# Kernel optimization log

Measured on AMD Instinct MI355X. Metric: run time of the kernel, lower is better.

## Reference

```python
import jax, jax.numpy as jnp
import numpy as np

D = 128; H = 4; HD = 32; K = 4; OUT = 2; COND = 6; FF = 256

def _ln(x, g, b):
    m = x.mean(-1, keepdims=True)
    v = ((x - m) ** 2).mean(-1, keepdims=True)
    return g * (x - m) * jax.lax.rsqrt(v + 1e-5) + b

def setup_inputs() -> dict:
    key = jax.random.key(0)
    ks = jax.random.split(key, 40)
    B, S = 4096, 128
    def w(k, shape, scale=0.05):
        return (jax.random.normal(k, shape, dtype=jnp.float32) * scale)
    inp = {
        'x': jax.random.normal(ks[0], (B, OUT, S), dtype=jnp.float32),
        'timesteps': jax.random.randint(ks[1], (B,), 0, 1000, dtype=jnp.int32),
        'conditions': jax.random.normal(ks[2], (B, S, COND), dtype=jnp.float32),
        # time embedding MLP: Linear(128->256), SiLU, Linear(256->128)
        't_w1': w(ks[3], (D, 2 * D)), 't_b1': jnp.zeros((2 * D,), jnp.float32),
        't_w2': w(ks[4], (2 * D, D)), 't_b2': jnp.zeros((D,), jnp.float32),
        # condition MLP: Linear(6->64), SiLU, Linear(64->128), SiLU
        'c_w1': w(ks[5], (COND, D // 2)), 'c_b1': jnp.zeros((D // 2,), jnp.float32),
        'c_w2': w(ks[6], (D // 2, D)), 'c_b2': jnp.zeros((D,), jnp.float32),
        # 2 transformer encoder layers (post-norm, relu FFN, dropout=0 eval)
        'attn_wqkv': w(ks[7], (2, D, 3 * D)), 'attn_bqkv': jnp.zeros((2, 3 * D), jnp.float32),
        'attn_wo': w(ks[8], (2, D, D)), 'attn_bo': jnp.zeros((2, D), jnp.float32),
        'ln1_g': jnp.ones((2, D), jnp.float32), 'ln1_b': jnp.zeros((2, D), jnp.float32),
        'ff_w1': w(ks[9], (2, D, FF)), 'ff_b1': jnp.zeros((2, FF), jnp.float32),
        'ff_w2': w(ks[10], (2, FF, D)), 'ff_b2': jnp.zeros((2, D), jnp.float32),
        'ln2_g': jnp.ones((2, D), jnp.float32), 'ln2_b': jnp.zeros((2, D), jnp.float32),
        # mixture weights net: Linear(256->128), SiLU, Linear(128->4), Softmax
        'mw_w1': w(ks[11], (2 * D, D)), 'mw_b1': jnp.zeros((D,), jnp.float32),
        'mw_w2': w(ks[12], (D, K)), 'mw_b2': jnp.zeros((K,), jnp.float32),
        # K student networks: Linear(2+256->128), Tanh, Linear(128->2)
        's_w1': w(ks[13], (K, OUT + 2 * D, D)), 's_b1': jnp.zeros((K, D), jnp.float32),
        's_w2': w(ks[14], (K, D, OUT)), 's_b2': jnp.zeros((K, OUT), jnp.float32),
    }
    return inp

def reference(x, timesteps, conditions, t_w1, t_b1, t_w2, t_b2, c_w1, c_b1, c_w2, c_b2,
              attn_wqkv, attn_bqkv, attn_wo, attn_bo, ln1_g, ln1_b, ff_w1, ff_b1,
              ff_w2, ff_b2, ln2_g, ln2_b, mw_w1, mw_b1, mw_w2, mw_b2,
              s_w1, s_b1, s_w2, s_b2):
    B, _, S = x.shape
    # sinusoidal time embedding
    half = D // 2
    freqs = jnp.exp(-jnp.log(jnp.float32(10000.0)) * jnp.arange(half, dtype=jnp.float32) / half)
    args = timesteps.astype(jnp.float32)[:, None] * freqs[None, :]
    te = jnp.concatenate([jnp.cos(args), jnp.sin(args)], axis=-1)            # [B, D]
    time_emb = jax.nn.silu(te @ t_w1 + t_b1) @ t_w2 + t_b2                   # [B, D]
    # condition embedding MLP
    h = jax.nn.silu(conditions @ c_w1 + c_b1)
    h = jax.nn.silu(h @ c_w2 + c_b2)                                          # [B, S, D]
    # 2-layer transformer encoder (post-norm)
    for l in range(2):
        qkv = h @ attn_wqkv[l] + attn_bqkv[l]                                 # [B, S, 3D]
        q, k, v = jnp.split(qkv, 3, axis=-1)
        q = q.reshape(B, S, H, HD); k = k.reshape(B, S, H, HD); v = v.reshape(B, S, H, HD)
        sc = jnp.einsum('bqhd,bkhd->bhqk', q, k) / jnp.sqrt(jnp.float32(HD))
        a = jax.nn.softmax(sc, axis=-1)
        o = jnp.einsum('bhqk,bkhd->bqhd', a, v).reshape(B, S, D)
        o = o @ attn_wo[l] + attn_bo[l]
        h = _ln(h + o, ln1_g[l], ln1_b[l])
        f = jax.nn.relu(h @ ff_w1[l] + ff_b1[l]) @ ff_w2[l] + ff_b2[l]
        h = _ln(h + f, ln2_g[l], ln2_b[l])
    cond_emb = h.mean(axis=1)                                                 # [B, D]
    combined = jnp.concatenate([time_emb, cond_emb], axis=-1)                 # [B, 2D]
    mw = jax.nn.softmax(jax.nn.silu(combined @ mw_w1 + mw_b1) @ mw_w2 + mw_b2, axis=-1)  # [B, K]
    # students over all seq positions (vectorized over original seq loop)
    xt = jnp.transpose(x, (0, 2, 1))                                          # [B, S, OUT]
    emb_bs = jnp.broadcast_to(combined[:, None, :], (B, S, 2 * D))
    inp = jnp.concatenate([xt, emb_bs], axis=-1)                              # [B, S, OUT+2D]
    hk = jnp.tanh(jnp.einsum('bsi,kio->bsko', inp, s_w1) + s_b1)              # [B, S, K, D]
    ok = jnp.einsum('bsko,koj->bskj', hk, s_w2) + s_b2                        # [B, S, K, OUT]
    out = jnp.einsum('bskj,bk->bsj', ok, mw)                                  # [B, S, OUT]
    return jnp.transpose(out, (0, 2, 1))                                      # [B, OUT, S]
```

## Files before the change

kernel.cpp:

```cpp
#include <hip/hip_runtime.h>

typedef _Float16 hf;
typedef _Float16 hf4 __attribute__((ext_vector_type(4)));
typedef _Float16 hf8 __attribute__((ext_vector_type(8)));
typedef float f4 __attribute__((ext_vector_type(4)));

#define NTH 512
#define ACT_OFF 0
#define P_OFF   32768
#define SC_OFF  40960
#define SMEM_BYTES 73728

#define WSH_QKV 0
#define WSH_WO  98304
#define WSH_FW1 131072
#define WSH_FW2 196608
#define WSH_CW2 262144
#define WSH_TOTAL 270336
#define CEMB_BYTE_OFF 540672

__device__ __forceinline__ float dsilu(float x){ return x / (1.f + __expf(-x)); }
__device__ __forceinline__ float dtanh(float x){
  float xc = fminf(fmaxf(x, -10.f), 10.f);
  float e = __expf(2.f * xc);
  return (e - 1.f) / (e + 1.f);
}

__global__ void prep_pack(const float* __restrict__ wqkv, const float* __restrict__ wo,
                          const float* __restrict__ fw1, const float* __restrict__ fw2,
                          const float* __restrict__ cw2, hf* __restrict__ ws){
  int idx = blockIdx.x * 256 + threadIdx.x;
  if (idx >= WSH_TOTAL) return;
  float v;
  if (idx < WSH_WO){
    int u = idx; int lh = u / 12288; int l = lh >> 2, h = lh & 3;
    int r = u % 12288; int tl = r >> 9; int lane = (r >> 3) & 63; int j = r & 7;
    int q = lane >> 4, c = lane & 15;
    int tn = tl >> 2, tk = tl & 3;
    int k = tk*32 + q*8 + j, nloc = tn*16 + c;
    int gcol = (nloc >> 5)*128 + h*32 + (nloc & 31);
    v = wqkv[l*49152 + k*384 + gcol];
  } else if (idx < WSH_FW1){
    int u = idx - WSH_WO; int l = u >> 14; int r = u & 16383;
    int tl = r >> 9; int lane = (r >> 3) & 63; int j = r & 7;
    int q = lane >> 4, c = lane & 15;
    int tn = tl >> 2, tk = tl & 3;
    v = wo[l*16384 + (tk*32 + q*8 + j)*128 + tn*16 + c];
  } else if (idx < WSH_FW2){
    int u = idx - WSH_FW1; int lch = u >> 14; int l = lch >> 1, ch = lch & 1; int r = u & 16383;
    int tl = r >> 9; int lane = (r >> 3) & 63; int j = r & 7;
    int q = lane >> 4, c = lane & 15;
    int tn = tl >> 2, tk = tl & 3;
    v = fw1[l*32768 + (tk*32 + q*8 + j)*256 + ch*128 + tn*16 + c];
  } else if (idx < WSH_CW2){
    int u = idx - WSH_FW2; int lch = u >> 14; int l = lch >> 1, ch = lch & 1; int r = u & 16383;
    int tl = r >> 9; int lane = (r >> 3) & 63; int j = r & 7;
    int q = lane >> 4, c = lane & 15;
    int tn = tl >> 2, tk = tl & 3;
    v = fw2[l*32768 + (ch*128 + tk*32 + q*8 + j)*128 + tn*16 + c];
  } else {
    int u = idx - WSH_CW2;
    int tl = u >> 9; int lane = (u >> 3) & 63; int j = u & 7;
    int q = lane >> 4, c = lane & 15;
    int tn = tl >> 1, tk = tl & 1;
    v = cw2[(tk*32 + q*8 + j)*128 + tn*16 + c];
  }
  ws[idx] = (hf)v;
}

template<int KT>
__device__ __forceinline__ void gemmB(f4 (&acc)[4][2], const hf* __restrict__ Ag, const hf* Bh,
                                      int npair, int shalf, int lane){
#pragma unroll
  for (int tk = 0; tk < KT; ++tk){
    hf8 a0 = *(const hf8*)(Ag + (((2*npair    )*KT + tk) << 9) + lane*8);
    hf8 a1 = *(const hf8*)(Ag + (((2*npair + 1)*KT + tk) << 9) + lane*8);
#pragma unroll
    for (int si = 0; si < 4; ++si){
      hf8 b = *(const hf8*)(Bh + (((shalf*4 + si)*KT + tk) << 9) + lane*8);
      acc[si][0] = __builtin_amdgcn_mfma_f32_16x16x32_f16(a0, b, acc[si][0], 0, 0, 0);
      acc[si][1] = __builtin_amdgcn_mfma_f32_16x16x32_f16(a1, b, acc[si][1], 0, 0, 0);
    }
  }
}

__device__ __forceinline__ void store_packed_b64(hf* dst, int KtilesOut, int ts, int ft,
                                                 f4 v, int q, int c){
  int tk = ft >> 1;
  int qp = ((ft & 1) << 1) + (q >> 1);
  int j0 = (q & 1) << 2;
  hf4 h; h[0] = (hf)v[0]; h[1] = (hf)v[1]; h[2] = (hf)v[2]; h[3] = (hf)v[3];
  *(hf4*)(dst + ((ts*KtilesOut + tk) << 9) + ((qp*16 + c) << 3) + j0) = h;
}

__device__ __forceinline__ void ln_pass(hf* A, const hf* Dh, const float* __restrict__ g,
                                        const float* __restrict__ bb, int t){
  int s = t >> 2, p = t & 3;
  float xr[4][8];
  int offs[4];
  float sum = 0.f, sq = 0.f;
#pragma unroll
  for (int tk = 0; tk < 4; ++tk){
    int off = (((s >> 4) * 4 + tk) << 9) + ((p * 16 + (s & 15)) << 3);
    offs[tk] = off;
    hf8 va = *(const hf8*)(A + off);
    hf8 vd = *(const hf8*)(Dh + off);
#pragma unroll
    for (int j = 0; j < 8; ++j){
      float x = (float)va[j] + (float)vd[j];
      xr[tk][j] = x; sum += x; sq += x * x;
    }
  }
  sum += __shfl_xor(sum, 1); sq += __shfl_xor(sq, 1);
  sum += __shfl_xor(sum, 2); sq += __shfl_xor(sq, 2);
  float mean = sum * (1.f/128.f);
  float rstd = rsqrtf(sq * (1.f/128.f) - mean*mean + 1e-5f);
#pragma unroll
  for (int tk = 0; tk < 4; ++tk){
    int f0 = tk*32 + p*8;
    f4 g0 = *(const f4*)(g + f0); f4 g1 = *(const f4*)(g + f0 + 4);
    f4 b0 = *(const f4*)(bb + f0); f4 b1 = *(const f4*)(bb + f0 + 4);
    hf8 y;
#pragma unroll
    for (int j = 0; j < 4; ++j){
      y[j]     = (hf)((xr[tk][j]     - mean) * rstd * g0[j] + b0[j]);
      y[j + 4] = (hf)((xr[tk][j + 4] - mean) * rstd * g1[j] + b1[j]);
    }
    *(hf8*)(A + offs[tk]) = y;
  }
}

__global__ __launch_bounds__(NTH, 4) void fused_fp(
    const float* __restrict__ cond,
    const float* __restrict__ c_w1, const float* __restrict__ c_b1, const float* __restrict__ c_b2,
    const float* __restrict__ bqkv_g, const float* __restrict__ bo_g,
    const float* __restrict__ ln1g_g, const float* __restrict__ ln1b_g,
    const float* __restrict__ fb1_g, const float* __restrict__ fb2_g,
    const float* __restrict__ ln2g_g, const float* __restrict__ ln2b_g,
    const hf* __restrict__ wsp, float* __restrict__ cemb)
{
  extern __shared__ char smem[];
  hf* ACTh = (hf*)(smem + ACT_OFF);
  hf* Ph   = (hf*)(smem + P_OFF);
  hf* SCh  = (hf*)(smem + SC_OFF);
  float* SCf = (float*)(smem + SC_OFF);
  hf* Qh  = SCh;
  hf* Kh  = (hf*)(smem + SC_OFF + 8192);
  hf* VTh = (hf*)(smem + SC_OFF + 16384);
  float* cst  = SCf + 4096;
  float* cw1s = SCf + 4864;

  const int b = blockIdx.x;
  const int t = threadIdx.x;
  const int w = t >> 6, lane = t & 63, q = lane >> 4, c = lane & 15;
  const int sp = w & 3, np = w >> 2;
  const int npair = w & 3, shalf = w >> 2;

  for (int idx = t; idx < 768; idx += NTH) cst[idx] = cond[b * 768 + idx];
  if (t < 384) cw1s[t] = c_w1[t];
  if (t < 64)  cw1s[384 + t] = c_b1[t];
  __syncthreads();

  for (int idx = t; idx < 8192; idx += NTH){
    int s = idx >> 6, jf = idx & 63;
    float a = cw1s[384 + jf];
#pragma unroll
    for (int cc = 0; cc < 6; ++cc) a += cst[s * 6 + cc] * cw1s[cc * 64 + jf];
    SCh[(((s >> 4)*2 + (jf >> 5)) << 9) + ((((jf & 31) >> 3)*16 + (s & 15)) << 3) + (jf & 7)] = (hf)dsilu(a);
  }
  __syncthreads();

  {
    f4 acc[4][2];
#pragma unroll
    for (int i = 0; i < 4; ++i)
#pragma unroll
      for (int j = 0; j < 2; ++j){ f4 z = {0.f,0.f,0.f,0.f}; acc[i][j] = z; }
    gemmB<2>(acc, wsp + WSH_CW2, SCh, npair, shalf, lane);
    f4 cb0 = *(const f4*)(c_b2 + (2*npair    )*16 + q*4);
    f4 cb1 = *(const f4*)(c_b2 + (2*npair + 1)*16 + q*4);
#pragma unroll
    for (int si = 0; si < 4; ++si)
#pragma unroll
      for (int jn = 0; jn < 2; ++jn){
        f4 v = acc[si][jn];
        f4 cb = jn ? cb1 : cb0;
#pragma unroll
        for (int r = 0; r < 4; ++r) v[r] = dsilu(v[r] + cb[r]);
        store_packed_b64(ACTh, 4, shalf*4 + si, 2*npair + jn, v, q, c);
      }
  }

  for (int l = 0; l < 2; ++l){
    f4 oacc[8];
#pragma unroll
    for (int i = 0; i < 8; ++i){ f4 z = {0.f,0.f,0.f,0.f}; oacc[i] = z; }

    for (int h = 0; h < 4; ++h){
      __syncthreads();
      {
        const hf* Aq = wsp + WSH_QKV + (l*4 + h)*12288;
        f4 acc[2][3];
#pragma unroll
        for (int i = 0; i < 2; ++i)
#pragma unroll
          for (int j = 0; j < 3; ++j){ f4 z = {0.f,0.f,0.f,0.f}; acc[i][j] = z; }
#pragma unroll
        for (int tk = 0; tk < 4; ++tk){
          hf8 b0 = *(const hf8*)(ACTh + (((2*sp  )*4 + tk) << 9) + lane*8);
          hf8 b1 = *(const hf8*)(ACTh + (((2*sp+1)*4 + tk) << 9) + lane*8);
#pragma unroll
          for (int jn = 0; jn < 3; ++jn){
            hf8 a = *(const hf8*)(Aq + (((np*3 + jn)*4 + tk) << 9) + lane*8);
            acc[0][jn] = __builtin_amdgcn_mfma_f32_16x16x32_f16(a, b0, acc[0][jn], 0, 0, 0);
            acc[1][jn] = __builtin_amdgcn_mfma_f32_16x16x32_f16(a, b1, acc[1][jn], 0, 0, 0);
          }
        }
#pragma unroll
        for (int si = 0; si < 2; ++si)
#pragma unroll
          for (int jn = 0; jn < 3; ++jn){
            int ft = np*3 + jn, ts = 2*sp + si;
            int sel = ft >> 1;
            f4 v = acc[si][jn];
            f4 bq = *(const f4*)(bqkv_g + l*384 + sel*128 + h*32 + (ft & 1)*16 + q*4);
#pragma unroll
            for (int r = 0; r < 4; ++r) v[r] += bq[r];
            if (sel == 0){
#pragma unroll
              for (int r = 0; r < 4; ++r) v[r] *= 0.17677669529663687f;
              store_packed_b64(Qh, 1, ts, ft, v, q, c);
            } else if (sel == 1){
              store_packed_b64(Kh, 1, ts, ft - 2, v, q, c);
            } else {
              int td = ft - 4;
              int qp = ((ts & 1) << 1) + (c >> 3);
              hf* pb = VTh + ((td*4 + (ts >> 1)) << 9) + (c & 7);
#pragma unroll
              for (int r = 0; r < 4; ++r) pb[(qp*16 + q*4 + r) << 3] = (hf)v[r];
            }
          }
      }
      __syncthreads();
      {
        hf8 qf = *(const hf8*)(Qh + (w << 9) + lane*8);
        f4 sc[8];
#pragma unroll
        for (int kst = 0; kst < 8; ++kst){
          hf8 kv = *(const hf8*)(Kh + (kst << 9) + lane*8);
          f4 z = {0.f,0.f,0.f,0.f};
          sc[kst] = __builtin_amdgcn_mfma_f32_16x16x32_f16(kv, qf, z, 0, 0, 0);
        }
        float ls = 0.f;
#pragma unroll
        for (int kst = 0; kst < 8; ++kst)
#pragma unroll
          for (int r = 0; r < 4; ++r){
            float e = __expf(sc[kst][r]);
            sc[kst][r] = e; ls += e;
          }
        ls += __shfl_xor(ls, 16);
        ls += __shfl_xor(ls, 32);
        float rl = 1.f / ls;
        hf* Pw = Ph + (w << 9);
#pragma unroll
        for (int ks = 0; ks < 4; ++ks){
#pragma unroll
          for (int h2 = 0; h2 < 2; ++h2){
            int kst = 2*ks + h2;
            int qp = h2*2 + (q >> 1);
            int j0 = (q & 1) << 2;
            hf4 pv;
#pragma unroll
            for (int r = 0; r < 4; ++r) pv[r] = (hf)(sc[kst][r] * rl);
            *(hf4*)(Pw + qp*128 + c*8 + j0) = pv;
          }
          hf8 bp = *(const hf8*)(Pw + lane*8);
          hf8 a0 = *(const hf8*)(VTh + ((     ks) << 9) + lane*8);
          hf8 a1 = *(const hf8*)(VTh + ((4 +  ks) << 9) + lane*8);
          oacc[2*h]     = __builtin_amdgcn_mfma_f32_16x16x32_f16(a0, bp, oacc[2*h],     0, 0, 0);
          oacc[2*h + 1] = __builtin_amdgcn_mfma_f32_16x16x32_f16(a1, bp, oacc[2*h + 1], 0, 0, 0);
        }
      }
    }

    __syncthreads();
#pragma unroll
    for (int ft = 0; ft < 8; ++ft) store_packed_b64(SCh, 4, w, ft, oacc[ft], q, c);
    __syncthreads();

    {
      f4 acc[4][2];
#pragma unroll
      for (int i = 0; i < 4; ++i)
#pragma unroll
        for (int j = 0; j < 2; ++j){ f4 z = {0.f,0.f,0.f,0.f}; acc[i][j] = z; }
      gemmB<4>(acc, wsp + WSH_WO + l*16384, SCh, npair, shalf, lane);
      __syncthreads();
      f4 bo0 = *(const f4*)(bo_g + l*128 + (2*npair    )*16 + q*4);
      f4 bo1 = *(const f4*)(bo_g + l*128 + (2*npair + 1)*16 + q*4);
#pragma unroll
      for (int si = 0; si < 4; ++si)
#pragma unroll
        for (int jn = 0; jn < 2; ++jn){
          f4 v = acc[si][jn];
          f4 bo = jn ? bo1 : bo0;
#pragma unroll
          for (int r = 0; r < 4; ++r) v[r] += bo[r];
          store_packed_b64(SCh, 4, shalf*4 + si, 2*npair + jn, v, q, c);
        }
    }
    __syncthreads();
    ln_pass(ACTh, SCh, ln1g_g + l*128, ln1b_g + l*128, t);
    __syncthreads();

    {
      f4 facc[4][2];
#pragma unroll
      for (int i = 0; i < 4; ++i)
#pragma unroll
        for (int j = 0; j < 2; ++j){ f4 z = {0.f,0.f,0.f,0.f}; facc[i][j] = z; }
      for (int ch = 0; ch < 2; ++ch){
        f4 acc[4][2];
#pragma unroll
        for (int i = 0; i < 4; ++i)
#pragma unroll
          for (int j = 0; j < 2; ++j){ f4 z = {0.f,0.f,0.f,0.f}; acc[i][j] = z; }
        gemmB<4>(acc, wsp + WSH_FW1 + (l*2 + ch)*16384, ACTh, npair, shalf, lane);
        f4 fb0 = *(const f4*)(fb1_g + l*256 + ch*128 + (2*npair    )*16 + q*4);
        f4 fb1v = *(const f4*)(fb1_g + l*256 + ch*128 + (2*npair + 1)*16 + q*4);
#pragma unroll
        for (int si = 0; si < 4; ++si)
#pragma unroll
          for (int jn = 0; jn < 2; ++jn){
            f4 v = acc[si][jn];
            f4 fb = jn ? fb1v : fb0;
#pragma unroll
            for (int r = 0; r < 4; ++r) v[r] = fmaxf(v[r] + fb[r], 0.f);
            store_packed_b64(SCh, 4, shalf*4 + si, 2*npair + jn, v, q, c);
          }
        __syncthreads();
        gemmB<4>(facc, wsp + WSH_FW2 + (l*2 + ch)*16384, SCh, npair, shalf, lane);
        __syncthreads();
      }
      f4 f20 = *(const f4*)(fb2_g + l*128 + (2*npair    )*16 + q*4);
      f4 f21 = *(const f4*)(fb2_g + l*128 + (2*npair + 1)*16 + q*4);
#pragma unroll
      for (int si = 0; si < 4; ++si)
#pragma unroll
        for (int jn = 0; jn < 2; ++jn){
          f4 v = facc[si][jn];
          f4 fb = jn ? f21 : f20;
#pragma unroll
          for (int r = 0; r < 4; ++r) v[r] += fb[r];
          store_packed_b64(SCh, 4, shalf*4 + si, 2*npair + jn, v, q, c);
        }
    }
    __syncthreads();
    ln_pass(ACTh, SCh, ln2g_g + l*128, ln2b_g + l*128, t);
    __syncthreads();
  }

  {
    int o = t & 15;
    float fs[8];
#pragma unroll
    for (int j = 0; j < 8; ++j) fs[j] = 0.f;
#pragma unroll
    for (int u = 0; u < 4; ++u){
      int s = (t >> 4)*4 + u;
      hf8 v = *(const hf8*)(ACTh + (((s >> 4)*4 + (o >> 2)) << 9) + (((o & 3)*16 + (s & 15)) << 3));
#pragma unroll
      for (int j = 0; j < 8; ++j) fs[j] += (float)v[j];
    }
#pragma unroll
    for (int j = 0; j < 8; ++j){
      fs[j] += __shfl_xor(fs[j], 16);
      fs[j] += __shfl_xor(fs[j], 32);
    }
    if (lane < 16){
      f4 v0, v1;
#pragma unroll
      for (int j = 0; j < 4; ++j){ v0[j] = fs[j]; v1[j] = fs[j+4]; }
      *(f4*)(SCf + w*128 + o*8)     = v0;
      *(f4*)(SCf + w*128 + o*8 + 4) = v1;
    }
  }
  __syncthreads();
  if (t < 128){
    float a = 0.f;
#pragma unroll
    for (int wv = 0; wv < 8; ++wv) a += SCf[wv*128 + t];
    cemb[b*128 + t] = a * (1.f/128.f);
  }
}

__global__ __launch_bounds__(256, 8) void tail_k(
    const float* __restrict__ x, const int* __restrict__ tstep, const float* __restrict__ cemb,
    const float* __restrict__ t_w1, const float* __restrict__ t_b1,
    const float* __restrict__ t_w2, const float* __restrict__ t_b2,
    const float* __restrict__ mw_w1, const float* __restrict__ mw_b1,
    const float* __restrict__ mw_w2, const float* __restrict__ mw_b2,
    const float* __restrict__ s_w1, const float* __restrict__ s_b1,
    const float* __restrict__ s_w2, const float* __restrict__ s_b2,
    float* __restrict__ out)
{
  __shared__ float sw01[1024], sw2[1024];
  __shared__ float comb[256];
  __shared__ float cvec[512];
  __shared__ float scr[1024];
  __shared__ float mwh[128], mwls[4];
  const int b = blockIdx.x;
  const int t = threadIdx.x;

  for (int i = t; i < 1024; i += 256){
    int row = i >> 9, k = (i >> 7) & 3, j = i & 127;
    sw01[i] = s_w1[k*33024 + row*128 + j];
    sw2[i]  = s_w2[i];
  }
  if (t < 128){
    int i = t & 63;
    float f = __expf(-logf(10000.f) * (float)i * (1.f/64.f));
    float a = (float)tstep[b] * f;
    cvec[t] = (t < 64) ? cosf(a) : sinf(a);
    comb[128 + t] = cemb[b*128 + t];
  }
  __syncthreads();

  {
    float a = t_b1[t];
#pragma unroll 8
    for (int i = 0; i < 128; ++i) a += cvec[i] * t_w1[i*256 + t];
    cvec[128 + t] = dsilu(a);
  }
  __syncthreads();

  {
    int ih = t >> 7, j = t & 127;
    float a = ih ? 0.f : t_b2[j];
#pragma unroll 8
    for (int ii = 0; ii < 128; ++ii){
      int i = ih*128 + ii;
      a += cvec[128 + i] * t_w2[i*128 + j];
    }
    scr[t] = a;
  }
  __syncthreads();
  if (t < 128) comb[t] = scr[t] + scr[128 + t];
  __syncthreads();

  {
    int ih = t >> 7, k = (t >> 5) & 3, j4 = t & 31;
    f4 a = {0.f, 0.f, 0.f, 0.f};
    const f4* wp = (const f4*)(s_w1 + k*33024 + 256 + ih*16384) + j4;
#pragma unroll 4
    for (int ii = 0; ii < 128; ++ii){
      float cb = comb[ih*128 + ii];
      f4 wv = wp[ii*32];
      a[0] += cb*wv[0]; a[1] += cb*wv[1]; a[2] += cb*wv[2]; a[3] += cb*wv[3];
    }
    ((f4*)scr)[ih*128 + k*32 + j4] = a;
  }
  __syncthreads();

  if (t < 128){
    f4 r0 = ((f4*)scr)[t];
    f4 r1 = ((f4*)scr)[128 + t];
    f4 r; r[0] = r0[0]+r1[0]; r[1] = r0[1]+r1[1]; r[2] = r0[2]+r1[2]; r[3] = r0[3]+r1[3];
    int k = t >> 5, j4 = t & 31;
    f4 sb = *(const f4*)(s_b1 + k*128 + j4*4);
    r[0] += sb[0]; r[1] += sb[1]; r[2] += sb[2]; r[3] += sb[3];
    ((f4*)cvec)[t] = r;
  } else {
    int j = t - 128;
    float a = mw_b1[j];
#pragma unroll 8
    for (int i = 0; i < 256; ++i) a += comb[i] * mw_w1[i*128 + j];
    mwh[j] = dsilu(a);
  }
  __syncthreads();

  if (t < 64){
    int cc = t & 3, j0 = t >> 2;
    float a = 0.f;
#pragma unroll
    for (int i = 0; i < 8; ++i){
      int j = j0 + 16*i;
      a += mwh[j] * mw_w2[j*4 + cc];
    }
    a += __shfl_xor(a, 4);
    a += __shfl_xor(a, 8);
    a += __shfl_xor(a, 16);
    a += __shfl_xor(a, 32);
    if (t < 4) mwls[t] = a + mw_b2[t];
  }
#pragma unroll
  for (int u = 0; u < 2; ++u){
    int o = t + u*256, k = o >> 7, s = o & 127;
    float x0 = x[b*256 + s];
    float x1 = x[b*256 + 128 + s];
    float a0 = 0.f, a1 = 0.f;
#pragma unroll 4
    for (int j = 0; j < 128; ++j){
      float hk = dtanh(cvec[k*128 + j] + x0*sw01[k*128 + j] + x1*sw01[512 + k*128 + j]);
      a0 += hk * sw2[k*256 + 2*j];
      a1 += hk * sw2[k*256 + 2*j + 1];
    }
    scr[k*256 + s]       = a0 + s_b2[2*k];
    scr[k*256 + 128 + s] = a1 + s_b2[2*k + 1];
  }
  __syncthreads();

  {
    int row = t >> 7, s = t & 127;
    float l0 = mwls[0], l1 = mwls[1], l2 = mwls[2], l3 = mwls[3];
    float mx = fmaxf(fmaxf(l0, l1), fmaxf(l2, l3));
    float e0 = __expf(l0 - mx), e1 = __expf(l1 - mx), e2 = __expf(l2 - mx), e3 = __expf(l3 - mx);
    float rs = 1.f / (e0 + e1 + e2 + e3);
    float a = e0*scr[0*256 + row*128 + s] + e1*scr[1*256 + row*128 + s]
            + e2*scr[2*256 + row*128 + s] + e3*scr[3*256 + row*128 + s];
    out[b*256 + row*128 + s] = a * rs;
  }
}

extern "C" void kernel_launch(void* const* d_in, const int* in_sizes, int n_in,
                              void* d_out, int out_size, void* d_ws, size_t ws_size,
                              hipStream_t stream){
  (void)n_in; (void)ws_size; (void)out_size;
  hipFuncSetAttribute((const void*)fused_fp, hipFuncAttributeMaxDynamicSharedMemorySize, SMEM_BYTES);
  int B = in_sizes[1];
  hf* wsp = (hf*)d_ws;
  float* cemb = (float*)((char*)d_ws + CEMB_BYTE_OFF);
  prep_pack<<<dim3((WSH_TOTAL + 255) / 256), dim3(256), 0, stream>>>(
      (const float*)d_in[11], (const float*)d_in[13], (const float*)d_in[17],
      (const float*)d_in[19], (const float*)d_in[9], wsp);
  fused_fp<<<dim3(B), dim3(NTH), SMEM_BYTES, stream>>>(
      (const float*)d_in[2],
      (const float*)d_in[7], (const float*)d_in[8], (const float*)d_in[10],
      (const float*)d_in[12], (const float*)d_in[14],
      (const float*)d_in[15], (const float*)d_in[16],
      (const float*)d_in[18], (const float*)d_in[20],
      (const float*)d_in[21], (const float*)d_in[22],
      wsp, cemb);
  tail_k<<<dim3(B), dim3(256), 0, stream>>>(
      (const float*)d_in[0], (const int*)d_in[1], cemb,
      (const float*)d_in[3], (const float*)d_in[4], (const float*)d_in[5], (const float*)d_in[6],
      (const float*)d_in[23], (const float*)d_in[24], (const float*)d_in[25], (const float*)d_in[26],
      (const float*)d_in[27], (const float*)d_in[28], (const float*)d_in[29], (const float*)d_in[30],
      (float*)d_out);
}
```

Baseline: 1.088 ms.

## Prefetch MFMA weight fragments before barriers and use fp16 dot2 in tail

In the fused transformer kernel, the global-memory weight fragments for each GEMM are loaded into registers before the preceding __syncthreads. This lets their latency overlap with the barrier wait, and the FFN chunk loop is unrolled so each chunk's loads are issued early. The tail kernel now reads fp16-prepacked time-MLP, mixture and student weights from a new prep kernel and accumulates with dot2 instructions. The student tanh loop is also vectorized with f4 shared-memory reads. This raises register pressure and lowers tail-path precision to fp16 inputs.

```diff
diff --git a/kernel.cpp b/kernel.cpp
--- a/kernel.cpp
+++ b/kernel.cpp
@@ -1,6 +1,7 @@
 #include <hip/hip_runtime.h>
 
 typedef _Float16 hf;
+typedef _Float16 hf2 __attribute__((ext_vector_type(2)));
 typedef _Float16 hf4 __attribute__((ext_vector_type(4)));
 typedef _Float16 hf8 __attribute__((ext_vector_type(8)));
 typedef float f4 __attribute__((ext_vector_type(4)));
@@ -18,12 +19,25 @@
 #define WSH_CW2 262144
 #define WSH_TOTAL 270336
 #define CEMB_BYTE_OFF 540672
+#define SP1_BYTE_OFF  2637824
+#define TPH_SW1 0
+#define TPH_TW1 131072
+#define TPH_TW2 163840
+#define TPH_MW1 196608
+#define TPH_TOTAL 229376
 
 __device__ __forceinline__ float dsilu(float x){ return x / (1.f + __expf(-x)); }
 __device__ __forceinline__ float dtanh(float x){
   float xc = fminf(fmaxf(x, -10.f), 10.f);
   float e = __expf(2.f * xc);
   return (e - 1.f) / (e + 1.f);
+}
+__device__ __forceinline__ float fdot2f(hf2 a, hf2 b, float c){
+#if __has_builtin(__builtin_amdgcn_fdot2)
+  return __builtin_amdgcn_fdot2(a, b, c, false);
+#else
+  return c + (float)a[0]*(float)b[0] + (float)a[1]*(float)b[1];
+#endif
 }
 
 __global__ void prep_pack(const float* __restrict__ wqkv, const float* __restrict__ wo,
@@ -68,18 +82,50 @@
   ws[idx] = (hf)v;
 }
 
+__global__ void prep_pack2(const float* __restrict__ s_w1, const float* __restrict__ t_w1,
+                           const float* __restrict__ t_w2, const float* __restrict__ mw_w1,
+                           hf* __restrict__ sp1){
+  int idx = blockIdx.x * 256 + threadIdx.x;
+  if (idx >= TPH_TOTAL) return;
+  float v;
+  if (idx < TPH_TW1){
+    int par = idx & 1, j = (idx >> 1) & 127, ip = (idx >> 8) & 127, k = idx >> 15;
+    v = s_w1[k*33024 + (2 + 2*ip + par)*128 + j];
+  } else if (idx < TPH_TW2){
+    int u = idx - TPH_TW1;
+    int par = u & 1, tc = (u >> 1) & 255, ip = u >> 9;
+    v = t_w1[(2*ip + par)*256 + tc];
+  } else if (idx < TPH_MW1){
+    int u = idx - TPH_TW2;
+    int par = u & 1, j = (u >> 1) & 127, ip = u >> 8;
+    v = t_w2[(2*ip + par)*128 + j];
+  } else {
+    int u = idx - TPH_MW1;
+    int par = u & 1, j = (u >> 1) & 127, ip = u >> 8;
+    v = mw_w1[(2*ip + par)*128 + j];
+  }
+  sp1[idx] = (hf)v;
+}
+
 template<int KT>
-__device__ __forceinline__ void gemmB(f4 (&acc)[4][2], const hf* __restrict__ Ag, const hf* Bh,
-                                      int npair, int shalf, int lane){
+__device__ __forceinline__ void loadA2(hf8 (&ar)[2][KT], const hf* __restrict__ Ag, int npair, int lane){
+#pragma unroll
+  for (int jn = 0; jn < 2; ++jn)
+#pragma unroll
+    for (int tk = 0; tk < KT; ++tk)
+      ar[jn][tk] = *(const hf8*)(Ag + (((2*npair + jn)*KT + tk) << 9) + lane*8);
+}
+
+template<int KT>
+__device__ __forceinline__ void gemmBpre(f4 (&acc)[4][2], const hf8 (&ar)[2][KT], const hf* Bh,
+                                         int shalf, int lane){
 #pragma unroll
   for (int tk = 0; tk < KT; ++tk){
-    hf8 a0 = *(const hf8*)(Ag + (((2*npair    )*KT + tk) << 9) + lane*8);
-    hf8 a1 = *(const hf8*)(Ag + (((2*npair + 1)*KT + tk) << 9) + lane*8);
 #pragma unroll
     for (int si = 0; si < 4; ++si){
       hf8 b = *(const hf8*)(Bh + (((shalf*4 + si)*KT + tk) << 9) + lane*8);
-      acc[si][0] = __builtin_amdgcn_mfma_f32_16x16x32_f16(a0, b, acc[si][0], 0, 0, 0);
-      acc[si][1] = __builtin_amdgcn_mfma_f32_16x16x32_f16(a1, b, acc[si][1], 0, 0, 0);
+      acc[si][0] = __builtin_amdgcn_mfma_f32_16x16x32_f16(ar[0][tk], b, acc[si][0], 0, 0, 0);
+      acc[si][1] = __builtin_amdgcn_mfma_f32_16x16x32_f16(ar[1][tk], b, acc[si][1], 0, 0, 0);
     }
   }
 }
@@ -168,15 +214,16 @@
     for (int cc = 0; cc < 6; ++cc) a += cst[s * 6 + cc] * cw1s[cc * 64 + jf];
     SCh[(((s >> 4)*2 + (jf >> 5)) << 9) + ((((jf & 31) >> 3)*16 + (s & 15)) << 3) + (jf & 7)] = (hf)dsilu(a);
   }
-  __syncthreads();
-
   {
+    hf8 acw[2][2];
+    loadA2<2>(acw, wsp + WSH_CW2, npair, lane);
+    __syncthreads();
     f4 acc[4][2];
 #pragma unroll
     for (int i = 0; i < 4; ++i)
 #pragma unroll
       for (int j = 0; j < 2; ++j){ f4 z = {0.f,0.f,0.f,0.f}; acc[i][j] = z; }
-    gemmB<2>(acc, wsp + WSH_CW2, SCh, npair, shalf, lane);
+    gemmBpre<2>(acc, acw, SCh, shalf, lane);
     f4 cb0 = *(const f4*)(c_b2 + (2*npair    )*16 + q*4);
     f4 cb1 = *(const f4*)(c_b2 + (2*npair + 1)*16 + q*4);
 #pragma unroll
@@ -197,9 +244,17 @@
     for (int i = 0; i < 8; ++i){ f4 z = {0.f,0.f,0.f,0.f}; oacc[i] = z; }
 
     for (int h = 0; h < 4; ++h){
-      __syncthreads();
+      hf8 aq[3][4];
       {
         const hf* Aq = wsp + WSH_QKV + (l*4 + h)*12288;
+#pragma unroll
+        for (int jn = 0; jn < 3; ++jn)
+#pragma unroll
+          for (int tk = 0; tk < 4; ++tk)
+            aq[jn][tk] = *(const hf8*)(Aq + (((np*3 + jn)*4 + tk) << 9) + lane*8);
+      }
+      __syncthreads();
+      {
         f4 acc[2][3];
 #pragma unroll
         for (int i = 0; i < 2; ++i)
@@ -211,9 +266,8 @@
           hf8 b1 = *(const hf8*)(ACTh + (((2*sp+1)*4 + tk) << 9) + lane*8);
 #pragma unroll
           for (int jn = 0; jn < 3; ++jn){
-            hf8 a = *(const hf8*)(Aq + (((np*3 + jn)*4 + tk) << 9) + lane*8);
-            acc[0][jn] = __builtin_amdgcn_mfma_f32_16x16x32_f16(a, b0, acc[0][jn], 0, 0, 0);
-            acc[1][jn] = __builtin_amdgcn_mfma_f32_16x16x32_f16(a, b1, acc[1][jn], 0, 0, 0);
+            acc[0][jn] = __builtin_amdgcn_mfma_f32_16x16x32_f16(aq[jn][tk], b0, acc[0][jn], 0, 0, 0);
+            acc[1][jn] = __builtin_amdgcn_mfma_f32_16x16x32_f16(aq[jn][tk], b1, acc[1][jn], 0, 0, 0);
           }
         }
 #pragma unroll
@@ -284,6 +338,8 @@
       }
     }
 
+    hf8 awo[2][4];
+    loadA2<4>(awo, wsp + WSH_WO + l*16384, npair, lane);
     __syncthreads();
 #pragma unroll
     for (int ft = 0; ft < 8; ++ft) store_packed_b64(SCh, 4, w, ft, oacc[ft], q, c);
@@ -295,7 +351,7 @@
       for (int i = 0; i < 4; ++i)
 #pragma unroll
         for (int j = 0; j < 2; ++j){ f4 z = {0.f,0.f,0.f,0.f}; acc[i][j] = z; }
-      gemmB<4>(acc, wsp + WSH_WO + l*16384, SCh, npair, shalf, lane);
+      gemmBpre<4>(acc, awo, SCh, shalf, lane);
       __syncthreads();
       f4 bo0 = *(const f4*)(bo_g + l*128 + (2*npair    )*16 + q*4);
       f4 bo1 = *(const f4*)(bo_g + l*128 + (2*npair + 1)*16 + q*4);
@@ -312,7 +368,6 @@
     }
     __syncthreads();
     ln_pass(ACTh, SCh, ln1g_g + l*128, ln1b_g + l*128, t);
-    __syncthreads();
 
     {
       f4 facc[4][2];
@@ -320,15 +375,18 @@
       for (int i = 0; i < 4; ++i)
 #pragma unroll
         for (int j = 0; j < 2; ++j){ f4 z = {0.f,0.f,0.f,0.f}; facc[i][j] = z; }
-      for (int ch = 0; ch < 2; ++ch){
+      hf8 af1[2][4], af2[2][4];
+      loadA2<4>(af1, wsp + WSH_FW1 + (l*2 + 0)*16384, npair, lane);
+      __syncthreads();
+      {
         f4 acc[4][2];
 #pragma unroll
         for (int i = 0; i < 4; ++i)
 #pragma unroll
           for (int j = 0; j < 2; ++j){ f4 z = {0.f,0.f,0.f,0.f}; acc[i][j] = z; }
-        gemmB<4>(acc, wsp + WSH_FW1 + (l*2 + ch)*16384, ACTh, npair, shalf, lane);
-        f4 fb0 = *(const f4*)(fb1_g + l*256 + ch*128 + (2*npair    )*16 + q*4);
-        f4 fb1v = *(const f4*)(fb1_g + l*256 + ch*128 + (2*npair + 1)*16 + q*4);
+        gemmBpre<4>(acc, af1, ACTh, shalf, lane);
+        f4 fb0 = *(const f4*)(fb1_g + l*256 + (2*npair    )*16 + q*4);
+        f4 fb1v = *(const f4*)(fb1_g + l*256 + (2*npair + 1)*16 + q*4);
 #pragma unroll
         for (int si = 0; si < 4; ++si)
 #pragma unroll
@@ -339,10 +397,36 @@
             for (int r = 0; r < 4; ++r) v[r] = fmaxf(v[r] + fb[r], 0.f);
             store_packed_b64(SCh, 4, shalf*4 + si, 2*npair + jn, v, q, c);
           }
-        __syncthreads();
-        gemmB<4>(facc, wsp + WSH_FW2 + (l*2 + ch)*16384, SCh, npair, shalf, lane);
-        __syncthreads();
       }
+      loadA2<4>(af2, wsp + WSH_FW2 + (l*2 + 0)*16384, npair, lane);
+      __syncthreads();
+      gemmBpre<4>(facc, af2, SCh, shalf, lane);
+      loadA2<4>(af1, wsp + WSH_FW1 + (l*2 + 1)*16384, npair, lane);
+      __syncthreads();
+      {
+        f4 acc[4][2];
+#pragma unroll
+        for (int i = 0; i < 4; ++i)
+#pragma unroll
+          for (int j = 0; j < 2; ++j){ f4 z = {0.f,0.f,0.f,0.f}; acc[i][j] = z; }
+        gemmBpre<4>(acc, af1, ACTh, shalf, lane);
+        f4 fb0 = *(const f4*)(fb1_g + l*256 + 128 + (2*npair    )*16 + q*4);
+        f4 fb1v = *(const f4*)(fb1_g + l*256 + 128 + (2*npair + 1)*16 + q*4);
+#pragma unroll
+        for (int si = 0; si < 4; ++si)
+#pragma unroll
+          for (int jn = 0; jn < 2; ++jn){
+            f4 v = acc[si][jn];
+            f4 fb = jn ? fb1v : fb0;
+#pragma unroll
+            for (int r = 0; r < 4; ++r) v[r] = fmaxf(v[r] + fb[r], 0.f);
+            store_packed_b64(SCh, 4, shalf*4 + si, 2*npair + jn, v, q, c);
+          }
+      }
+      loadA2<4>(af2, wsp + WSH_FW2 + (l*2 + 1)*16384, npair, lane);
+      __syncthreads();
+      gemmBpre<4>(facc, af2, SCh, shalf, lane);
+      __syncthreads();
       f4 f20 = *(const f4*)(fb2_g + l*128 + (2*npair    )*16 + q*4);
       f4 f21 = *(const f4*)(fb2_g + l*128 + (2*npair + 1)*16 + q*4);
 #pragma unroll
@@ -397,19 +481,18 @@
 
 __global__ __launch_bounds__(256, 8) void tail_k(
     const float* __restrict__ x, const int* __restrict__ tstep, const float* __restrict__ cemb,
-    const float* __restrict__ t_w1, const float* __restrict__ t_b1,
-    const float* __restrict__ t_w2, const float* __restrict__ t_b2,
-    const float* __restrict__ mw_w1, const float* __restrict__ mw_b1,
+    const float* __restrict__ t_b1, const float* __restrict__ t_b2,
+    const float* __restrict__ mw_b1,
     const float* __restrict__ mw_w2, const float* __restrict__ mw_b2,
     const float* __restrict__ s_w1, const float* __restrict__ s_b1,
     const float* __restrict__ s_w2, const float* __restrict__ s_b2,
-    float* __restrict__ out)
+    const hf* __restrict__ sp1, float* __restrict__ out)
 {
   __shared__ float sw01[1024], sw2[1024];
-  __shared__ float comb[256];
   __shared__ float cvec[512];
   __shared__ float scr[1024];
   __shared__ float mwh[128], mwls[4];
+  __shared__ hf te_h[128], th_h[256], comb_h[256];
   const int b = blockIdx.x;
   const int t = threadIdx.x;
 
@@ -422,42 +505,57 @@
     int i = t & 63;
     float f = __expf(-logf(10000.f) * (float)i * (1.f/64.f));
     float a = (float)tstep[b] * f;
-    cvec[t] = (t < 64) ? cosf(a) : sinf(a);
-    comb[128 + t] = cemb[b*128 + t];
+    te_h[t] = (hf)((t < 64) ? cosf(a) : sinf(a));
+    comb_h[128 + t] = (hf)cemb[b*128 + t];
   }
   __syncthreads();
 
   {
+    const hf* tp1 = sp1 + TPH_TW1;
     float a = t_b1[t];
 #pragma unroll 8
-    for (int i = 0; i < 128; ++i) a += cvec[i] * t_w1[i*256 + t];
-    cvec[128 + t] = dsilu(a);
+    for (int ii = 0; ii < 64; ++ii){
+      hf2 wp = *(const hf2*)(tp1 + ii*512 + 2*t);
+      hf2 tp = *(const hf2*)(te_h + 2*ii);
+      a = fdot2f(tp, wp, a);
+    }
+    th_h[t] = (hf)dsilu(a);
   }
   __syncthreads();
 
   {
+    const hf* tp2 = sp1 + TPH_TW2;
     int ih = t >> 7, j = t & 127;
     float a = ih ? 0.f : t_b2[j];
 #pragma unroll 8
-    for (int ii = 0; ii < 128; ++ii){
-      int i = ih*128 + ii;
-      a += cvec[128 + i] * t_w2[i*128 + j];
+    for (int ii = 0; ii < 64; ++ii){
+      hf2 wp = *(const hf2*)(tp2 + (ih*64 + ii)*256 + 2*j);
+      hf2 tp = *(const hf2*)(th_h + ih*128 + 2*ii);
+      a = fdot2f(tp, wp, a);
     }
     scr[t] = a;
   }
   __syncthreads();
-  if (t < 128) comb[t] = scr[t] + scr[128 + t];
+  if (t < 128) comb_h[t] = (hf)(scr[t] + scr[128 + t]);
   __syncthreads();
 
   {
+    const hf* swp = sp1 + TPH_SW1;
     int ih = t >> 7, k = (t >> 5) & 3, j4 = t & 31;
     f4 a = {0.f, 0.f, 0.f, 0.f};
-    const f4* wp = (const f4*)(s_w1 + k*33024 + 256 + ih*16384) + j4;
+    const hf* wp = swp + ((k*128 + ih*64)*128 + j4*4)*2;
 #pragma unroll 4
-    for (int ii = 0; ii < 128; ++ii){
-      float cb = comb[ih*128 + ii];
-      f4 wv = wp[ii*32];
-      a[0] += cb*wv[0]; a[1] += cb*wv[1]; a[2] += cb*wv[2]; a[3] += cb*wv[3];
+    for (int ii = 0; ii < 64; ++ii){
+      hf8 wv = *(const hf8*)(wp + ii*256);
+      hf2 cb = *(const hf2*)(comb_h + ih*128 + 2*ii);
+      hf2 w01; w01[0] = wv[0]; w01[1] = wv[1];
+      hf2 w23; w23[0] = wv[2]; w23[1] = wv[3];
+      hf2 w45; w45[0] = wv[4]; w45[1] = wv[5];
+      hf2 w67; w67[0] = wv[6]; w67[1] = wv[7];
+      a[0] = fdot2f(cb, w01, a[0]);
+      a[1] = fdot2f(cb, w23, a[1]);
+      a[2] = fdot2f(cb, w45, a[2]);
+      a[3] = fdot2f(cb, w67, a[3]);
     }
     ((f4*)scr)[ih*128 + k*32 + j4] = a;
   }
@@ -466,16 +564,21 @@
   if (t < 128){
     f4 r0 = ((f4*)scr)[t];
     f4 r1 = ((f4*)scr)[128 + t];
-    f4 r; r[0] = r0[0]+r1[0]; r[1] = r0[1]+r1[1]; r[2] = r0[2]+r1[2]; r[3] = r0[3]+r1[3];
     int k = t >> 5, j4 = t & 31;
     f4 sb = *(const f4*)(s_b1 + k*128 + j4*4);
-    r[0] += sb[0]; r[1] += sb[1]; r[2] += sb[2]; r[3] += sb[3];
+    f4 r; r[0] = r0[0]+r1[0]+sb[0]; r[1] = r0[1]+r1[1]+sb[1];
+    r[2] = r0[2]+r1[2]+sb[2]; r[3] = r0[3]+r1[3]+sb[3];
     ((f4*)cvec)[t] = r;
   } else {
+    const hf* mp1 = sp1 + TPH_MW1;
     int j = t - 128;
     float a = mw_b1[j];
 #pragma unroll 8
-    for (int i = 0; i < 256; ++i) a += comb[i] * mw_w1[i*128 + j];
+    for (int ii = 0; ii < 128; ++ii){
+      hf2 wp = *(const hf2*)(mp1 + ii*256 + 2*j);
+      hf2 cp = *(const hf2*)(comb_h + 2*ii);
+      a = fdot2f(cp, wp, a);
+    }
     mwh[j] = dsilu(a);
   }
   __syncthreads();
@@ -500,11 +603,20 @@
     float x0 = x[b*256 + s];
     float x1 = x[b*256 + 128 + s];
     float a0 = 0.f, a1 = 0.f;
-#pragma unroll 4
-    for (int j = 0; j < 128; ++j){
-      float hk = dtanh(cvec[k*128 + j] + x0*sw01[k*128 + j] + x1*sw01[512 + k*128 + j]);
-      a0 += hk * sw2[k*256 + 2*j];
-      a1 += hk * sw2[k*256 + 2*j + 1];
+    const f4* cvp = (const f4*)cvec + k*32;
+    const f4* w0p = (const f4*)sw01 + k*32;
+    const f4* w1p = (const f4*)sw01 + 128 + k*32;
+    const f4* s2p = (const f4*)sw2 + k*64;
+#pragma unroll 2
+    for (int j4 = 0; j4 < 32; ++j4){
+      f4 cv = cvp[j4], w0 = w0p[j4], w1 = w1p[j4];
+      f4 s20 = s2p[2*j4], s21 = s2p[2*j4 + 1];
+      float h0 = dtanh(cv[0] + x0*w0[0] + x1*w1[0]);
+      float h1 = dtanh(cv[1] + x0*w0[1] + x1*w1[1]);
+      float h2 = dtanh(cv[2] + x0*w0[2] + x1*w1[2]);
+      float h3 = dtanh(cv[3] + x0*w0[3] + x1*w1[3]);
+      a0 += h0*s20[0] + h1*s20[2] + h2*s21[0] + h3*s21[2];
+      a1 += h0*s20[1] + h1*s20[3] + h2*s21[1] + h3*s21[3];
     }
     scr[k*256 + s]       = a0 + s_b2[2*k];
     scr[k*256 + 128 + s] = a1 + s_b2[2*k + 1];
@@ -531,9 +643,13 @@
   int B = in_sizes[1];
   hf* wsp = (hf*)d_ws;
   float* cemb = (float*)((char*)d_ws + CEMB_BYTE_OFF);
+  hf* sp1 = (hf*)((char*)d_ws + SP1_BYTE_OFF);
   prep_pack<<<dim3((WSH_TOTAL + 255) / 256), dim3(256), 0, stream>>>(
       (const float*)d_in[11], (const float*)d_in[13], (const float*)d_in[17],
       (const float*)d_in[19], (const float*)d_in[9], wsp);
+  prep_pack2<<<dim3((TPH_TOTAL + 255) / 256), dim3(256), 0, stream>>>(
+      (const float*)d_in[27], (const float*)d_in[3], (const float*)d_in[5],
+      (const float*)d_in[23], sp1);
   fused_fp<<<dim3(B), dim3(NTH), SMEM_BYTES, stream>>>(
       (const float*)d_in[2],
       (const float*)d_in[7], (const float*)d_in[8], (const float*)d_in[10],
@@ -544,8 +660,9 @@
       wsp, cemb);
   tail_k<<<dim3(B), dim3(256), 0, stream>>>(
       (const float*)d_in[0], (const int*)d_in[1], cemb,
-      (const float*)d_in[3], (const float*)d_in[4], (const float*)d_in[5], (const float*)d_in[6],
-      (const float*)d_in[23], (const float*)d_in[24], (const float*)d_in[25], (const float*)d_in[26],
+      (const float*)d_in[4], (const float*)d_in[6],
+      (const float*)d_in[24],
+      (const float*)d_in[25], (const float*)d_in[26],
       (const float*)d_in[27], (const float*)d_in[28], (const float*)d_in[29], (const float*)d_in[30],
-      (float*)d_out);
-}
+      sp1, (float*)d_out);
+}
```

New measurement: 1.053 ms. 1.03x faster.
